# Kernel optimization log

Measured on AMD Instinct MI355X. Metric: run time of the kernel, lower is better.

Reference implementation:

```python
import jax, jax.numpy as jnp
import numpy as np
import itertools

N, F, R, O, OUT = 131072, 32, 256, 5, 100
K = 9  # 2*exp_param + 1 with exp_param=4


def setup_inputs() -> dict:
    key = jax.random.key(0)
    k1, k2, k3 = jax.random.split(key, 3)
    # binary features -> get_route(x)==1 -> categorical rule path
    x = jax.random.randint(k1, (N, F), 0, 2).astype(jnp.float32)
    # first R combinations of O feature indices out of F (itertools order, as in __init__)
    combs = np.array(list(itertools.islice(itertools.combinations(range(F), O), R)), dtype=np.int32)
    comb_space = jax.random.normal(k2, (O, R), dtype=jnp.float32)
    w_out = jax.random.normal(k3, (OUT, R), dtype=jnp.float32) * 0.05
    b_out = jnp.zeros((OUT,), jnp.float32)
    return {"x": x, "comb_space": comb_space, "w_out": w_out, "b_out": b_out,
            "comb_idx": jnp.asarray(combs)}


def reference(x, comb_space, w_out, b_out, comb_idx):
    # Fused version of the per-rule Python loop:
    # gather all rule feature subsets at once: [N, R, O]
    gathered = x[:, comb_idx]
    # per-rule dot product with its parameter vector comb_space[:, r]
    scores = jnp.einsum('nro,or->nr', gathered, comb_space)  # [N, R]
    # polyClip activation: clamp(s^k, -1, 1)
    comb_pred = jnp.clip(scores ** K, -1.0, 1.0)
    # dropout p=0.1 is identity in eval mode
    attn = jax.nn.softmax(comb_pred, axis=1)                 # [N, R]
    out = attn @ w_out.T + b_out                             # [N, OUT]
    return jax.nn.log_softmax(out, axis=1)
```

## Files before the change

kernel.cpp:

```cpp
#include <hip/hip_runtime.h>

typedef unsigned short u16;
typedef _Float16 f16;
typedef __attribute__((ext_vector_type(2))) __fp16 hf16x2;
typedef __attribute__((ext_vector_type(4))) _Float16 f16x4;
typedef __attribute__((ext_vector_type(8))) _Float16 f16x8;
typedef __attribute__((ext_vector_type(4))) float f32x4;

#define N_ROWS 131072
#define FDIM 32
#define RDIM 256
#define ODIM 5
#define NOUT 100
#define JT 7
#define WAVES 8
#define ROWS_PER_BLOCK (WAVES * 2 * 16)
#define NBLOCKS (N_ROWS / ROWS_PER_BLOCK)

#define MF_SLOTS 1024
#define WF_SLOTS (JT * 8 * 64)
#define TAB_SLOTS (MF_SLOTS + WF_SLOTS)

#define CSCALE 1.04156363f
#define CLIP2  1.44269504f

typedef const __attribute__((address_space(1))) void gvoid;
typedef __attribute__((address_space(3))) void lvoid;

__device__ __forceinline__ u16 f2h_bits(float f) {
    f16 h = (f16)f;
    union { f16 h; u16 u; } v; v.h = h;
    return v.u;
}

__global__ void build_tabs(const float* __restrict__ cs, const float* __restrict__ w,
                           const int* __restrict__ ci, u16* __restrict__ tabs) {
    int t = blockIdx.x * 256 + threadIdx.x;
    if (t >= TAB_SLOTS) return;
    u16 vals[8];
    if (t < MF_SLOTS) {
        int l = t & 63, rt = t >> 6;
        int r = rt * 16 + (l & 15);
        int kbase = (l >> 4) * 8;
        int idx0 = ci[r * ODIM + 0], idx1 = ci[r * ODIM + 1], idx2 = ci[r * ODIM + 2];
        int idx3 = ci[r * ODIM + 3], idx4 = ci[r * ODIM + 4];
#pragma unroll
        for (int e = 0; e < 8; ++e) {
            int k = kbase + e;
            float v = 0.f;
            if (idx0 == k) v = cs[0 * RDIM + r];
            if (idx1 == k) v = cs[1 * RDIM + r];
            if (idx2 == k) v = cs[2 * RDIM + r];
            if (idx3 == k) v = cs[3 * RDIM + r];
            if (idx4 == k) v = cs[4 * RDIM + r];
            vals[e] = f2h_bits(v * CSCALE);
        }
    } else {
        int s = t - MF_SLOTS;
        int l = s & 63, ft = s >> 6;
        int jt = ft >> 3, rtp = ft & 7;
        int j = jt * 16 + (l & 15);
        if (j < NOUT) {
            const float* wp = w + (size_t)j * RDIM + rtp * 32 + (l >> 4) * 4;
            float4 va = *(const float4*)wp;
            float4 vb = *(const float4*)(wp + 16);
            vals[0] = f2h_bits(va.x); vals[1] = f2h_bits(va.y);
            vals[2] = f2h_bits(va.z); vals[3] = f2h_bits(va.w);
            vals[4] = f2h_bits(vb.x); vals[5] = f2h_bits(vb.y);
            vals[6] = f2h_bits(vb.z); vals[7] = f2h_bits(vb.w);
        } else {
            u16 fill = (j == NOUT) ? f2h_bits(1.0f) : (u16)0;
#pragma unroll
            for (int e = 0; e < 8; ++e) vals[e] = fill;
        }
    }
    *(uint4*)(tabs + (size_t)t * 8) = *(const uint4*)vals;
}

__device__ __forceinline__ f16x4 elemop(f32x4 cc) {
    float ev[4];
#pragma unroll
    for (int i = 0; i < 4; ++i) {
        float s = cc[i];
        float s2 = s * s, s4 = s2 * s2, s8 = s4 * s4;
        float p = __builtin_amdgcn_fmed3f(s8 * s, -CLIP2, CLIP2);
        float e;
        asm("v_exp_f32 %0, %1" : "=v"(e) : "v"(p));
        ev[i] = e;
    }
    union { hf16x2 h; unsigned u; } lo, hi;
    lo.h = __builtin_amdgcn_cvt_pkrtz(ev[0], ev[1]);
    hi.h = __builtin_amdgcn_cvt_pkrtz(ev[2], ev[3]);
    union { unsigned u[2]; f16x4 v; } r;
    r.u[0] = lo.u; r.u[1] = hi.u;
    return r.v;
}

__device__ __forceinline__ void epilogue2(
    const f32x4* acc0, const f32x4* acc1, const float* bv,
    int rowb0, int c15, int g, float* __restrict__ out)
{
    float rin0[4], rin1[4];
#pragma unroll
    for (int i = 0; i < 4; ++i) {
        rin0[i] = __builtin_amdgcn_rcpf(__shfl(acc0[6][i], g * 16 + 4, 64));
        rin1[i] = __builtin_amdgcn_rcpf(__shfl(acc1[6][i], g * 16 + 4, 64));
    }
    const bool v6 = (c15 < 4);
#pragma unroll
    for (int i = 0; i < 4; ++i) {
        float lg0[JT], lg1[JT];
        float se0 = 0.f, se1 = 0.f;
#pragma unroll
        for (int jt = 0; jt < 6; ++jt) {
            lg0[jt] = fmaf(acc0[jt][i], rin0[i], bv[jt]);
            lg1[jt] = fmaf(acc1[jt][i], rin1[i], bv[jt]);
            se0 += __expf(lg0[jt]);
            se1 += __expf(lg1[jt]);
        }
        lg0[6] = fmaf(acc0[6][i], rin0[i], bv[6]);
        lg1[6] = fmaf(acc1[6][i], rin1[i], bv[6]);
        se0 += v6 ? __expf(lg0[6]) : 0.f;
        se1 += v6 ? __expf(lg1[6]) : 0.f;
#pragma unroll
        for (int m = 1; m <= 8; m <<= 1) {
            se0 += __shfl_xor(se0, m, 64);
            se1 += __shfl_xor(se1, m, 64);
        }
        float lse0 = __logf(se0), lse1 = __logf(se1);
        int row0 = rowb0 + g * 4 + i;
        float* op0 = out + (size_t)row0 * NOUT;
        float* op1 = op0 + 16 * NOUT;
#pragma unroll
        for (int jt = 0; jt < 6; ++jt) {
            op0[jt * 16 + c15] = lg0[jt] - lse0;
            op1[jt * 16 + c15] = lg1[jt] - lse1;
        }
        if (v6) {
            op0[96 + c15] = lg0[6] - lse0;
            op1[96 + c15] = lg1[6] - lse1;
        }
    }
}

__global__ __launch_bounds__(WAVES * 64, 2) void hornet_main(
    const float* __restrict__ x, const u16* __restrict__ tabs,
    const float* __restrict__ b_out, float* __restrict__ out)
{
    __shared__ __align__(16) u16 tab[TAB_SLOTS * 8];

    const int tid = threadIdx.x;
    const int lane = tid & 63;
    const int wid = tid >> 6;
    const int c15 = lane & 15, g = lane >> 4;

    const int rowb0 = blockIdx.x * ROWS_PER_BLOCK + wid * 32;
    const float* xp0 = x + (size_t)(rowb0 + c15) * FDIM + g * 8;
    float4 x0a = ((const float4*)xp0)[0];
    float4 x0b = ((const float4*)xp0)[1];
    float4 x1a = ((const float4*)(xp0 + 16 * FDIM))[0];
    float4 x1b = ((const float4*)(xp0 + 16 * FDIM))[1];

#pragma unroll
    for (int i = 0; i < 9; ++i) {
        const u16* gp = tabs + (size_t)(tid + i * 512) * 8;
        u16* lp = tab + (size_t)(wid * 64 + i * 512) * 8;
        __builtin_amdgcn_global_load_lds((gvoid*)gp, (lvoid*)lp, 16, 0, 0);
    }

    f16x8 a1_0, a1_1;
    a1_0[0] = (f16)x0a.x; a1_0[1] = (f16)x0a.y; a1_0[2] = (f16)x0a.z; a1_0[3] = (f16)x0a.w;
    a1_0[4] = (f16)x0b.x; a1_0[5] = (f16)x0b.y; a1_0[6] = (f16)x0b.z; a1_0[7] = (f16)x0b.w;
    a1_1[0] = (f16)x1a.x; a1_1[1] = (f16)x1a.y; a1_1[2] = (f16)x1a.z; a1_1[3] = (f16)x1a.w;
    a1_1[4] = (f16)x1b.x; a1_1[5] = (f16)x1b.y; a1_1[6] = (f16)x1b.z; a1_1[7] = (f16)x1b.w;

    __syncthreads();

    const f16x8* mfv = (const f16x8*)tab;
    const f16x8* wfv = (const f16x8*)(tab + MF_SLOTS * 8);

    f32x4 acc0[JT], acc1[JT];
#pragma unroll
    for (int jt = 0; jt < JT; ++jt) {
        acc0[jt] = (f32x4){0.f, 0.f, 0.f, 0.f};
        acc1[jt] = (f32x4){0.f, 0.f, 0.f, 0.f};
    }

    f16x8 b1a = mfv[lane];
    f16x8 b1b = mfv[64 + lane];

#pragma unroll 1
    for (int rtp = 0; rtp < 8; ++rtp) {
        f16x8 ca = b1a, cb = b1b;
        int nrtp = (rtp + 1) & 7;
        b1a = mfv[(2 * nrtp) * 64 + lane];
        b1b = mfv[(2 * nrtp + 1) * 64 + lane];

        const f32x4 z = {0.f, 0.f, 0.f, 0.f};
        __builtin_amdgcn_s_setprio(1);
        f32x4 cc0a = __builtin_amdgcn_mfma_f32_16x16x32_f16(ca, a1_0, z, 0, 0, 0);
        f32x4 cc0b = __builtin_amdgcn_mfma_f32_16x16x32_f16(cb, a1_0, z, 0, 0, 0);
        f32x4 cc1a = __builtin_amdgcn_mfma_f32_16x16x32_f16(ca, a1_1, z, 0, 0, 0);
        f32x4 cc1b = __builtin_amdgcn_mfma_f32_16x16x32_f16(cb, a1_1, z, 0, 0, 0);
        __builtin_amdgcn_s_setprio(0);

        f16x4 a2lo0 = elemop(cc0a);
        f16x4 a2hi0 = elemop(cc0b);
        f16x4 a2lo1 = elemop(cc1a);
        f16x4 a2hi1 = elemop(cc1b);

        const f16x8* wrow = wfv + rtp * 64 + lane;
        __builtin_amdgcn_s_setprio(1);
#pragma unroll
        for (int jt = 0; jt < JT; ++jt) {
            f16x8 b2 = wrow[jt * 8 * 64];
            f16x4 b2lo = __builtin_shufflevector(b2, b2, 0, 1, 2, 3);
            f16x4 b2hi = __builtin_shufflevector(b2, b2, 4, 5, 6, 7);
            acc0[jt] = __builtin_amdgcn_mfma_f32_16x16x16f16(a2lo0, b2lo, acc0[jt], 0, 0, 0);
            acc0[jt] = __builtin_amdgcn_mfma_f32_16x16x16f16(a2hi0, b2hi, acc0[jt], 0, 0, 0);
            acc1[jt] = __builtin_amdgcn_mfma_f32_16x16x16f16(a2lo1, b2lo, acc1[jt], 0, 0, 0);
            acc1[jt] = __builtin_amdgcn_mfma_f32_16x16x16f16(a2hi1, b2hi, acc1[jt], 0, 0, 0);
        }
        __builtin_amdgcn_s_setprio(0);
    }

    float bv[JT];
#pragma unroll
    for (int jt = 0; jt < JT; ++jt) {
        int j = jt * 16 + c15;
        bv[jt] = (j < NOUT) ? b_out[j] : 0.f;
    }

    epilogue2(acc0, acc1, bv, rowb0, c15, g, out);
}

extern "C" void kernel_launch(void* const* d_in, const int* in_sizes, int n_in,
                              void* d_out, int out_size, void* d_ws, size_t ws_size,
                              hipStream_t stream) {
    const float* x  = (const float*)d_in[0];
    const float* cs = (const float*)d_in[1];
    const float* w  = (const float*)d_in[2];
    const float* b  = (const float*)d_in[3];
    const int*   ci = (const int*)d_in[4];

    u16* tabs = (u16*)d_ws;

    hipLaunchKernelGGL(build_tabs, dim3(18), dim3(256), 0, stream, cs, w, ci, tabs);
    hipLaunchKernelGGL(hornet_main, dim3(NBLOCKS), dim3(WAVES * 64), 0, stream,
                       x, tabs, b, (float*)d_out);
}
```

Baseline: 31.42 us.

## Compute pow9-clip-exp in packed fp16 and read score table from global

Replaces the per-element fp32 power, clamp and exp with packed fp16 operations: v_pk_mul_f16 for s^9, pk max/min for the clip, and v_exp_f16 per half, with a perm to repack. This halves the VALU work in the elementwise stage between the two MFMA stages. Separately, the first-stage B-operand table is no longer staged in LDS but loaded directly from global memory, which shrinks LDS use and the initial copy. The fp16 power of the score may overflow or lose precision, and the global reads sit inside the loop with only one iteration of prefetch.

```diff
diff --git a/kernel.cpp b/kernel.cpp
--- a/kernel.cpp
+++ b/kernel.cpp
@@ -1,6 +1,7 @@
 #include <hip/hip_runtime.h>
 
 typedef unsigned short u16;
+typedef unsigned int u32;
 typedef _Float16 f16;
 typedef __attribute__((ext_vector_type(2))) __fp16 hf16x2;
 typedef __attribute__((ext_vector_type(4))) _Float16 f16x4;
@@ -77,22 +78,28 @@
     *(uint4*)(tabs + (size_t)t * 8) = *(const uint4*)vals;
 }
 
-__device__ __forceinline__ f16x4 elemop(f32x4 cc) {
-    float ev[4];
-#pragma unroll
-    for (int i = 0; i < 4; ++i) {
-        float s = cc[i];
-        float s2 = s * s, s4 = s2 * s2, s8 = s4 * s4;
-        float p = __builtin_amdgcn_fmed3f(s8 * s, -CLIP2, CLIP2);
-        float e;
-        asm("v_exp_f32 %0, %1" : "=v"(e) : "v"(p));
-        ev[i] = e;
-    }
-    union { hf16x2 h; unsigned u; } lo, hi;
-    lo.h = __builtin_amdgcn_cvt_pkrtz(ev[0], ev[1]);
-    hi.h = __builtin_amdgcn_cvt_pkrtz(ev[2], ev[3]);
-    union { unsigned u[2]; f16x4 v; } r;
-    r.u[0] = lo.u; r.u[1] = hi.u;
+__device__ __forceinline__ u32 pk_pow9_clip_exp(u32 h, u32 cpos, u32 cneg, u32 psel) {
+    u32 h2, h4, h8, p, phi, elo, ehi, r;
+    asm("v_pk_mul_f16 %0, %1, %1" : "=v"(h2) : "v"(h));
+    asm("v_pk_mul_f16 %0, %1, %1" : "=v"(h4) : "v"(h2));
+    asm("v_pk_mul_f16 %0, %1, %1" : "=v"(h8) : "v"(h4));
+    asm("v_pk_mul_f16 %0, %1, %2" : "=v"(p) : "v"(h8), "v"(h));
+    asm("v_pk_max_f16 %0, %1, %2" : "=v"(p) : "v"(p), "v"(cneg));
+    asm("v_pk_min_f16 %0, %1, %2" : "=v"(p) : "v"(p), "v"(cpos));
+    asm("v_lshrrev_b32 %0, 16, %1" : "=v"(phi) : "v"(p));
+    asm("v_exp_f16 %0, %1" : "=v"(elo) : "v"(p));
+    asm("v_exp_f16 %0, %1" : "=v"(ehi) : "v"(phi));
+    asm("v_perm_b32 %0, %1, %2, %3" : "=v"(r) : "v"(ehi), "v"(elo), "v"(psel));
+    return r;
+}
+
+__device__ __forceinline__ f16x4 elemop(f32x4 cc, u32 cpos, u32 cneg, u32 psel) {
+    union { hf16x2 h; u32 u; } h01, h23;
+    h01.h = __builtin_amdgcn_cvt_pkrtz(cc[0], cc[1]);
+    h23.h = __builtin_amdgcn_cvt_pkrtz(cc[2], cc[3]);
+    union { u32 u[2]; f16x4 v; } r;
+    r.u[0] = pk_pow9_clip_exp(h01.u, cpos, cneg, psel);
+    r.u[1] = pk_pow9_clip_exp(h23.u, cpos, cneg, psel);
     return r.v;
 }
 
@@ -147,7 +154,7 @@
     const float* __restrict__ x, const u16* __restrict__ tabs,
     const float* __restrict__ b_out, float* __restrict__ out)
 {
-    __shared__ __align__(16) u16 tab[TAB_SLOTS * 8];
+    __shared__ __align__(16) u16 tab[WF_SLOTS * 8];
 
     const int tid = threadIdx.x;
     const int lane = tid & 63;
@@ -162,8 +169,8 @@
     float4 x1b = ((const float4*)(xp0 + 16 * FDIM))[1];
 
 #pragma unroll
-    for (int i = 0; i < 9; ++i) {
-        const u16* gp = tabs + (size_t)(tid + i * 512) * 8;
+    for (int i = 0; i < 7; ++i) {
+        const u16* gp = tabs + (size_t)(MF_SLOTS + tid + i * 512) * 8;
         u16* lp = tab + (size_t)(wid * 64 + i * 512) * 8;
         __builtin_amdgcn_global_load_lds((gvoid*)gp, (lvoid*)lp, 16, 0, 0);
     }
@@ -174,10 +181,14 @@
     a1_1[0] = (f16)x1a.x; a1_1[1] = (f16)x1a.y; a1_1[2] = (f16)x1a.z; a1_1[3] = (f16)x1a.w;
     a1_1[4] = (f16)x1b.x; a1_1[5] = (f16)x1b.y; a1_1[6] = (f16)x1b.z; a1_1[7] = (f16)x1b.w;
 
+    const u32 cpos = 0x3DC53DC5u;
+    const u32 cneg = 0xBDC5BDC5u;
+    const u32 psel = 0x05040100u;
+
     __syncthreads();
 
-    const f16x8* mfv = (const f16x8*)tab;
-    const f16x8* wfv = (const f16x8*)(tab + MF_SLOTS * 8);
+    const f16x8* mfv = (const f16x8*)tabs;
+    const f16x8* wfv = (const f16x8*)tab;
 
     f32x4 acc0[JT], acc1[JT];
 #pragma unroll
@@ -204,10 +215,10 @@
         f32x4 cc1b = __builtin_amdgcn_mfma_f32_16x16x32_f16(cb, a1_1, z, 0, 0, 0);
         __builtin_amdgcn_s_setprio(0);
 
-        f16x4 a2lo0 = elemop(cc0a);
-        f16x4 a2hi0 = elemop(cc0b);
-        f16x4 a2lo1 = elemop(cc1a);
-        f16x4 a2hi1 = elemop(cc1b);
+        f16x4 a2lo0 = elemop(cc0a, cpos, cneg, psel);
+        f16x4 a2hi0 = elemop(cc0b, cpos, cneg, psel);
+        f16x4 a2lo1 = elemop(cc1a, cpos, cneg, psel);
+        f16x4 a2hi1 = elemop(cc1b, cpos, cneg, psel);
 
         const f16x8* wrow = wfv + rtp * 64 + lane;
         __builtin_amdgcn_s_setprio(1);
```

Measured after the change: 31.45 us. About the same (+0.1%).
